# Performance work log

Hardware: AMD Instinct MI355X
Metric: run time of the kernel (lower is better)

Reference implementation:

```python
import jax, jax.numpy as jnp
import numpy as np

B, S, D = 4, 2048, 768
H = 12
DH = D // H
NUM_WAY = 4
DFF = 4 * D  # FFN expansion scale=4
EPS = 1e-6


def setup_inputs() -> dict:
    key = jax.random.key(0)
    ks = jax.random.split(key, 20)
    s = 0.02
    inp = {
        "x": jax.random.normal(ks[0], (B, S, D), jnp.float32),
        "w": jax.random.randint(ks[1], (B, S), 0, NUM_WAY, jnp.int64),
        # LayerNorm 1
        "ln1_g": jnp.ones((D,), jnp.float32),
        "ln1_b": jnp.zeros((D,), jnp.float32),
        # Multi-head attention projections (input_dim=out_dim=D)
        "wq": jax.random.normal(ks[2], (D, D), jnp.float32) * s,
        "bq": jnp.zeros((D,), jnp.float32),
        "wk": jax.random.normal(ks[3], (D, D), jnp.float32) * s,
        "bk": jnp.zeros((D,), jnp.float32),
        "wv": jax.random.normal(ks[4], (D, D), jnp.float32) * s,
        "bv": jnp.zeros((D,), jnp.float32),
        "wo": jax.random.normal(ks[5], (D, D), jnp.float32) * s,
        "bo": jnp.zeros((D,), jnp.float32),
        # Way classifier
        "wcls": jax.random.normal(ks[6], (D, NUM_WAY), jnp.float32) * s,
        "bcls": jnp.zeros((NUM_WAY,), jnp.float32),
        # num_way stacked FFN experts: Linear(D,4D) -> ReLU -> Linear(4D,D)
        "w1": jax.random.normal(ks[7], (NUM_WAY, D, DFF), jnp.float32) * s,
        "b1": jnp.zeros((NUM_WAY, DFF), jnp.float32),
        "w2": jax.random.normal(ks[8], (NUM_WAY, DFF, D), jnp.float32) * s,
        "b2": jnp.zeros((NUM_WAY, D), jnp.float32),
    }
    return inp


def _layernorm(x, g, b):
    mu = jnp.mean(x, axis=-1, keepdims=True)
    var = jnp.mean(jnp.square(x - mu), axis=-1, keepdims=True)
    return (x - mu) * jax.lax.rsqrt(var + EPS) * g + b


def reference(x, w, ln1_g, ln1_b, wq, bq, wk, bk, wv, bv, wo, bo,
              wcls, bcls, w1, b1, w2, b2):
    # pre-LN
    xn = _layernorm(x, ln1_g, ln1_b)
    # multi-head self-attention (q = k = v = xn)
    q = (xn @ wq + bq).reshape(B, S, H, DH)
    k = (xn @ wk + bk).reshape(B, S, H, DH)
    v = (xn @ wv + bv).reshape(B, S, H, DH)
    scores = jnp.einsum('bqhd,bkhd->bhqk', q, k) / jnp.sqrt(jnp.float32(DH))
    attn = jax.nn.softmax(scores, axis=-1)
    ctx = jnp.einsum('bhqk,bkhd->bqhd', attn, v).reshape(B, S, D)
    ctx = ctx @ wo + bo
    # dropout is identity at inference; residual
    out = ctx + x
    # dense compute-all-experts FFN, then per-token select by routing id w
    # (mask-overwrite in original == one-hot select since masks partition)
    ffn_out = jnp.zeros_like(out)
    for ci in range(NUM_WAY):
        h = jax.nn.relu(out @ w1[ci] + b1[ci])        # [B,S,4D]
        fi = h @ w2[ci] + b2[ci]                      # [B,S,D]
        mask = (w == ci).astype(out.dtype)[..., None]  # [B,S,1]
        if ci == 0:
            # original initializes ffn_out with way-0 output everywhere;
            # later ways overwrite where w == ci, net = select expert w
            ffn_out = fi
        else:
            ffn_out = ffn_out * (1.0 - mask) + fi * mask
    way_logits = out @ wcls + bcls  # [B,S,NUM_WAY]
    return ffn_out, way_logits
```

## Files before the change

### kernel.cpp

```cpp
#include <hip/hip_runtime.h>
#include <cstdint>

typedef unsigned short u16;
typedef float f32x4 __attribute__((ext_vector_type(4)));
typedef float f32x16 __attribute__((ext_vector_type(16)));
typedef __bf16 bf16x8 __attribute__((ext_vector_type(8)));

#define LOG2E 1.44269504088896340736f

__device__ __forceinline__ u16 f2bf(float f) {
    union { float f; unsigned u; } v; v.f = f;
    unsigned r = v.u + 0x7fffu + ((v.u >> 16) & 1u);
    return (u16)(r >> 16);
}

__device__ __forceinline__ float bf2f(u16 v) {
    union { unsigned u; float f; } x; x.u = ((unsigned)v) << 16; return x.f;
}

__device__ __forceinline__ unsigned cvt_pk_bf16(float lo, float hi) {
    unsigned r;
    asm("v_cvt_pk_bf16_f32 %0, %1, %2" : "=v"(r) : "v"(lo), "v"(hi));
    return r;
}

__device__ __forceinline__ float exp2_hw(float x) {
    float r;
    asm("v_exp_f32 %0, %1" : "=v"(r) : "v"(x));
    return r;
}

__device__ __forceinline__ f32x4 mfma16(bf16x8 a, bf16x8 b, f32x4 c) {
    return __builtin_amdgcn_mfma_f32_16x16x32_bf16(a, b, c, 0, 0, 0);
}

__device__ __forceinline__ f32x16 mfma32(bf16x8 a, bf16x8 b, f32x16 c) {
    return __builtin_amdgcn_mfma_f32_32x32x16_bf16(a, b, c, 0, 0, 0);
}

__device__ __forceinline__ void gload_lds16(const void* g, void* l) {
    __builtin_amdgcn_global_load_lds(
        (__attribute__((address_space(1))) unsigned int*)(g),
        (__attribute__((address_space(3))) unsigned int*)(l),
        16, 0, 0);
}

#define MB_TOK 8192
#define DM 768
#define HH 12
#define DHD 64
#define NWAY 4
#define DFF 3072
#define SEQ 2048
#define NBATCH 4

#define PREP_LN_END   8192
#define PREP_T7_END   10496
#define PREP_W1_END   19712
#define PREP_W2_END   28928
#define PREP_CB_END   28937
#define PREP_GRID     28938

__global__ __launch_bounds__(256) void prep_kernel(
    const float* __restrict__ x, const float* __restrict__ ln_g,
    const float* __restrict__ ln_b, u16* __restrict__ xn,
    const float* __restrict__ wq, const float* __restrict__ wk,
    const float* __restrict__ wvv, const float* __restrict__ wo,
    u16* __restrict__ wqkvt, u16* __restrict__ wot,
    const float* __restrict__ w1, u16* __restrict__ w1t,
    const float* __restrict__ w2, u16* __restrict__ w2t,
    const float* __restrict__ bq, const float* __restrict__ bk,
    const float* __restrict__ bv, float* __restrict__ bqkv,
    const int* __restrict__ wl, int* __restrict__ perm,
    int* __restrict__ eoff, int4* __restrict__ fmap, int4* __restrict__ fmap64)
{
    __shared__ float tl[32][33];
    __shared__ float red[4];
    __shared__ int cnt[4], cur[4], off[5];
    int bid = blockIdx.x, tid = threadIdx.x;

    if (bid < PREP_LN_END) {
        int row = bid;
        const float* xr = x + (size_t)row * DM;
        float v0 = xr[tid], v1 = xr[tid + 256], v2 = xr[tid + 512];
        float s = v0 + v1 + v2;
        #pragma unroll
        for (int k = 1; k < 64; k <<= 1) s += __shfl_xor(s, k);
        if ((tid & 63) == 0) red[tid >> 6] = s;
        __syncthreads();
        float mu = (red[0] + red[1] + red[2] + red[3]) * (1.f / 768.f);
        float d0 = v0 - mu, d1 = v1 - mu, d2 = v2 - mu;
        float q = d0 * d0 + d1 * d1 + d2 * d2;
        #pragma unroll
        for (int k = 1; k < 64; k <<= 1) q += __shfl_xor(q, k);
        __syncthreads();
        if ((tid & 63) == 0) red[tid >> 6] = q;
        __syncthreads();
        float var = (red[0] + red[1] + red[2] + red[3]) * (1.f / 768.f);
        float rs = rsqrtf(var + 1e-6f);
        u16* xo = xn + (size_t)row * DM;
        xo[tid]       = f2bf(d0 * rs * ln_g[tid]       + ln_b[tid]);
        xo[tid + 256] = f2bf(d1 * rs * ln_g[tid + 256] + ln_b[tid + 256]);
        xo[tid + 512] = f2bf(d2 * rs * ln_g[tid + 512] + ln_b[tid + 512]);
        return;
    }
    if (bid < PREP_W2_END) {
        const float* src; u16* dst; int K, N, n0, k0;
        if (bid < PREP_T7_END) {
            int r = bid - PREP_LN_END;
            int wsel = r / 576, lb = r % 576;
            K = 768; N = 768;
            n0 = (lb % 24) * 32; k0 = (lb / 24) * 32;
            src = wsel == 0 ? wq : (wsel == 1 ? wk : (wsel == 2 ? wvv : wo));
            dst = wsel == 3 ? wot : (wqkvt + (size_t)wsel * 768 * 768);
        } else if (bid < PREP_W1_END) {
            int lb = bid - PREP_T7_END;
            K = 768; N = 3072;
            n0 = (lb % 96) * 32; k0 = ((lb / 96) % 24) * 32;
            int z = lb / 2304;
            src = w1 + (size_t)z * K * N; dst = w1t + (size_t)z * K * N;
        } else {
            int lb = bid - PREP_W1_END;
            K = 3072; N = 768;
            n0 = (lb % 24) * 32; k0 = ((lb / 24) % 96) * 32;
            int z = lb / 2304;
            src = w2 + (size_t)z * K * N; dst = w2t + (size_t)z * K * N;
        }
        int tx = tid & 31, ty = tid >> 5;
        #pragma unroll
        for (int j = 0; j < 4; ++j)
            tl[ty + j * 8][tx] = src[(size_t)(k0 + ty + j * 8) * N + n0 + tx];
        __syncthreads();
        #pragma unroll
        for (int j = 0; j < 4; ++j)
            dst[(size_t)(n0 + ty + j * 8) * K + k0 + tx] = f2bf(tl[tx][ty + j * 8]);
        return;
    }
    if (bid < PREP_CB_END) {
        int i = (bid - PREP_W2_END) * 256 + tid;
        if (i < 2304)
            bqkv[i] = i < 768 ? bq[i] : (i < 1536 ? bk[i - 768] : bv[i - 1536]);
        return;
    }
    if (tid < 4) cnt[tid] = 0;
    __syncthreads();
    for (int t = tid; t < MB_TOK; t += 256) atomicAdd(&cnt[wl[t] & 3], 1);
    __syncthreads();
    if (tid == 0) {
        off[0] = 0;
        for (int e = 0; e < 4; ++e) off[e + 1] = off[e] + cnt[e];
        int idx = 0;
        for (int e = 0; e < 4; ++e)
            for (int s = 0; s < cnt[e]; s += 128)
                fmap[idx++] = make_int4(e, off[e], s, cnt[e] - s);
        for (; idx < 72; ++idx) fmap[idx] = make_int4(-1, 0, 0, 0);
        int idx2 = 0;
        for (int e = 0; e < 4; ++e)
            for (int s = 0; s < cnt[e]; s += 64)
                fmap64[idx2++] = make_int4(e, off[e], s, cnt[e] - s);
        for (; idx2 < 136; ++idx2) fmap64[idx2] = make_int4(-1, 0, 0, 0);
        for (int e = 0; e < 5; ++e) eoff[e] = off[e];
        for (int e = 0; e < 4; ++e) cur[e] = off[e];
    }
    __syncthreads();
    for (int t = tid; t < MB_TOK; t += 256) {
        int e = wl[t] & 3;
        int pos = atomicAdd(&cur[e], 1);
        perm[pos] = t;
    }
}

__global__ __launch_bounds__(256) void vT_kernel(
    const u16* __restrict__ qkv, u16* __restrict__ vT)
{
    __shared__ u16 tl[32][33];
    int bh = blockIdx.z;
    int b = bh / HH, h = bh % HH;
    int key0 = blockIdx.x * 32;
    int d0 = blockIdx.y * 32;
    int tx = threadIdx.x & 31, ty = threadIdx.x >> 5;
    const u16* src = qkv + ((size_t)b * SEQ + key0) * 2304 + 1536 + h * 64 + d0;
    #pragma unroll
    for (int j = 0; j < 4; ++j)
        tl[ty + j * 8][tx] = src[(size_t)(ty + j * 8) * 2304 + tx];
    __syncthreads();
    u16* dst = vT + ((size_t)bh * 64 + d0) * SEQ + key0;
    #pragma unroll
    for (int j = 0; j < 4; ++j)
        dst[(size_t)(ty + j * 8) * SEQ + tx] = tl[tx][ty + j * 8];
}

template<int MODE, int TM, bool RELU, bool RES, bool ST32, bool ST16>
__global__ __launch_bounds__(256, 4) void gemm_bt_kernel(
    const u16* __restrict__ A, const u16* __restrict__ Bt,
    const float* __restrict__ bias, const float* __restrict__ res,
    float* __restrict__ out32, u16* __restrict__ out16,
    int nbt, int N, int K, int ntn,
    const int* __restrict__ perm, const int4* __restrict__ fmap)
{
    constexpr int ALD = TM * 32;
    constexpr int NN  = (TM == 64) ? 2 : 4;
    __shared__ __attribute__((aligned(16))) u16 As[2][ALD];
    __shared__ __attribute__((aligned(16))) u16 Bs[2][4096];
    int tid = threadIdx.x;
    int wv = tid >> 6, ln = tid & 63;
    int bpx = gridDim.x / (ntn << 3);
    int jj = blockIdx.x >> 3;
    int bt = (blockIdx.x & 7) * bpx + jj / ntn;
    int tn = (jj % ntn) * 128;
    if (bt >= nbt) return;

    int seg = 0, ms = 0, mb = TM, tm = 0;
    if (MODE != 0) {
        int4 ent = fmap[bt];
        if (ent.x < 0) return;
        seg = ent.y; ms = ent.z; mb = ent.w; if (mb > TM) mb = TM;
        Bt += (size_t)ent.x * N * K;
        bias += ent.x * N;
    } else {
        tm = bt * TM;
    }

    f32x4 acc[4][NN];
    #pragma unroll
    for (int i = 0; i < 4; ++i)
        #pragma unroll
        for (int j = 0; j < NN; ++j) acc[i][j] = f32x4{0.f, 0.f, 0.f, 0.f};

    int wr = (TM == 128) ? (wv >> 1) : 0;
    int wcol0 = (TM == 128) ? (wv & 1) * 64 : wv * 32;
    int lr = ln & 15, hi = ln >> 4;
    int nk = K / 32;

    const u16* asrc[2];
    const u16* bsrc[2];
    #pragma unroll
    for (int i = 0; i < 2; ++i) {
        int rA = (TM == 128) ? ((wv * 2 + i) * 16 + (ln >> 2))
                             : (wv * 16 + (ln >> 2));
        if (TM == 128 || i == 0) {
            int am = rA < mb ? rA : (mb - 1);
            size_t arow;
            if (MODE == 1)      arow = (size_t)perm[seg + ms + am];
            else if (MODE == 2) arow = (size_t)(seg + ms + am);
            else                arow = (size_t)(tm + rA);
            asrc[i] = A + arow * K + (ln & 3) * 8;
        }
        int rB = (wv * 2 + i) * 16 + (ln >> 2);
        bsrc[i] = Bt + (size_t)(tn + rB) * K + (ln & 3) * 8;
    }
    int aofs0 = (TM == 128) ? (wv * 2) * 512 : wv * 512;

#define GSTAGE(bf_, k0_) do {                                             \
    gload_lds16(asrc[0] + (k0_), &As[bf_][aofs0]);                        \
    if (TM == 128) gload_lds16(asrc[1] + (k0_), &As[bf_][aofs0 + 512]);   \
    gload_lds16(bsrc[0] + (k0_), &Bs[bf_][(wv * 2) * 512]);               \
    gload_lds16(bsrc[1] + (k0_), &Bs[bf_][(wv * 2 + 1) * 512]);           \
} while (0)

    GSTAGE(0, 0);
    for (int kk = 0; kk < nk; ++kk) {
        int bf = kk & 1;
        __syncthreads();
        if (kk + 1 < nk) GSTAGE(bf ^ 1, (kk + 1) * 32);
        bf16x8 a[4], b[NN];
        #pragma unroll
        for (int m = 0; m < 4; ++m)
            a[m] = *(const bf16x8*)&As[bf][(wr * 64 + m * 16 + lr) * 32 + hi * 8];
        #pragma unroll
        for (int n = 0; n < NN; ++n)
            b[n] = *(const bf16x8*)&Bs[bf][(wcol0 + n * 16 + lr) * 32 + hi * 8];
        #pragma unroll
        for (int m = 0; m < 4; ++m)
            #pragma unroll
            for (int n = 0; n < NN; ++n)
                acc[m][n] = mfma16(a[m], b[n], acc[m][n]);
    }
#undef GSTAGE

    #pragma unroll
    for (int m = 0; m < 4; ++m) {
        int rb = wr * 64 + m * 16 + hi * 4;
        #pragma unroll
        for (int n = 0; n < NN; ++n) {
            int gcol = tn + wcol0 + n * 16 + lr;
            float bvv = bias[gcol];
            #pragma unroll
            for (int i = 0; i < 4; ++i) {
                int rml = rb + i;
                float v = acc[m][n][i] + bvv;
                if (RELU) v = v > 0.f ? v : 0.f;
                if (MODE == 0) {
                    size_t grow = (size_t)(tm + rml);
                    if (RES) v += res[grow * N + gcol];
                    if (ST32) out32[grow * N + gcol] = v;
                    if (ST16) out16[grow * N + gcol] = f2bf(v);
                } else {
                    if (rml < mb) {
                        size_t orow = (MODE == 1) ? (size_t)(seg + ms + rml)
                                                  : (size_t)perm[seg + ms + rml];
                        if (ST32) out32[orow * N + gcol] = v;
                        if (ST16) out16[orow * N + gcol] = f2bf(v);
                    }
                }
            }
        }
    }
}

__global__ __launch_bounds__(256, 4) void attn_kernel(
    const u16* __restrict__ qkv, const u16* __restrict__ vT,
    u16* __restrict__ ctx)
{
    __shared__ __attribute__((aligned(16))) u16 Ks[2][4096];
    __shared__ __attribute__((aligned(16))) u16 Vs[2][4096];
    int tid = threadIdx.x;
    int wv = tid >> 6, ln = tid & 63;
    int qv = ln & 31, hi = ln >> 5;
    int bid = blockIdx.x;
    int bh = (bid & 7) * 6 + ((bid >> 3) % 6);
    int qt = (bid >> 3) / 6;
    int b = bh / HH, h = bh % HH;
    int q0 = qt * 128 + wv * 32;
    size_t qrowb = (size_t)(b * SEQ + q0);
    const float C = 0.125f * LOG2E;

    bf16x8 qf[4];
    {
        const u16* qp = qkv + (qrowb + qv) * 2304 + h * 64 + hi * 8;
        #pragma unroll
        for (int ds = 0; ds < 4; ++ds) qf[ds] = *(const bf16x8*)(qp + ds * 16);
    }

    int csrc = 8 * ((ln & 7) ^ (ln >> 3));
    const size_t kbase = (size_t)b * SEQ * 2304 + 768 + h * 64;
    const u16* vtb = vT + (size_t)bh * 64 * SEQ;
    const u16* kp0 = qkv + kbase + (size_t)(wv * 16 + (ln >> 3)) * 2304 + csrc;
    const u16* kp1 = kp0 + (size_t)8 * 2304;
    const u16* vp0 = vtb + (size_t)(wv * 16 + (ln >> 3)) * SEQ + csrc;
    const u16* vp1 = vp0 + (size_t)8 * SEQ;

#define ATTN_STAGE(bf_, t_) do {                                          \
    gload_lds16(kp0 + (size_t)(t_) * 64 * 2304, &Ks[bf_][(wv * 2) * 512]);\
    gload_lds16(kp1 + (size_t)(t_) * 64 * 2304, &Ks[bf_][(wv * 2 + 1) * 512]);\
    gload_lds16(vp0 + (size_t)(t_) * 64, &Vs[bf_][(wv * 2) * 512]);       \
    gload_lds16(vp1 + (size_t)(t_) * 64, &Vs[bf_][(wv * 2 + 1) * 512]);   \
} while (0)

    f32x16 oacc[2];
    #pragma unroll
    for (int i = 0; i < 2; ++i)
        #pragma unroll
        for (int r = 0; r < 16; ++r) oacc[i][r] = 0.f;
    float m_run = -INFINITY, l_run = 0.f;
    int ksw = (qv & 7) * 8;

    ATTN_STAGE(0, 0);

    for (int kt = 0; kt < SEQ / 64; ++kt) {
        int bf = kt & 1;
        __syncthreads();
        if (kt + 1 < SEQ / 64) ATTN_STAGE(bf ^ 1, kt + 1);

        f32x16 s0, s1;
        #pragma unroll
        for (int r = 0; r < 16; ++r) { s0[r] = 0.f; s1[r] = 0.f; }
        #pragma unroll
        for (int ds = 0; ds < 4; ++ds) {
            bf16x8 ka0 = *(const bf16x8*)&Ks[bf][qv * 64 + ((ds * 16 + hi * 8) ^ ksw)];
            bf16x8 ka1 = *(const bf16x8*)&Ks[bf][(32 + qv) * 64 + ((ds * 16 + hi * 8) ^ ksw)];
            s0 = mfma32(ka0, qf[ds], s0);
            s1 = mfma32(ka1, qf[ds], s1);
        }

        float tmax = s0[0];
        #pragma unroll
        for (int r = 1; r < 16; ++r) tmax = fmaxf(tmax, s0[r]);
        #pragma unroll
        for (int r = 0; r < 16; ++r) tmax = fmaxf(tmax, s1[r]);
        tmax = fmaxf(tmax, __shfl_xor(tmax, 32));

        if (!__all(tmax - m_run <= 64.f)) {
            float m_new = fmaxf(m_run, tmax);
            float corr = exp2_hw((m_run - m_new) * C);
            l_run *= corr;
            #pragma unroll
            for (int i = 0; i < 2; ++i)
                #pragma unroll
                for (int r = 0; r < 16; ++r) oacc[i][r] *= corr;
            m_run = m_new;
        }
        float c2 = -m_run * C;
        float psum = 0.f;
        #pragma unroll
        for (int r = 0; r < 16; ++r) {
            s0[r] = exp2_hw(fmaf(s0[r], C, c2)); psum += s0[r];
            s1[r] = exp2_hw(fmaf(s1[r], C, c2)); psum += s1[r];
        }
        l_run += psum;

        #pragma unroll
        for (int kb = 0; kb < 2; ++kb) {
            #pragma unroll
            for (int hc = 0; hc < 2; ++hc) {
                const f32x16& sv = kb ? s1 : s0;
                unsigned x0 = cvt_pk_bf16(sv[8 * hc + 0], sv[8 * hc + 1]);
                unsigned x1 = cvt_pk_bf16(sv[8 * hc + 2], sv[8 * hc + 3]);
                unsigned x2 = cvt_pk_bf16(sv[8 * hc + 4], sv[8 * hc + 5]);
                unsigned x3 = cvt_pk_bf16(sv[8 * hc + 6], sv[8 * hc + 7]);
                unsigned t0 = hi ? x0 : x2, t1 = hi ? x1 : x3;
                unsigned r0 = (unsigned)__shfl_xor((int)t0, 32);
                unsigned r1 = (unsigned)__shfl_xor((int)t1, 32);
                union { bf16x8 v; unsigned u[4]; } pf;
                pf.u[0] = hi ? r0 : x0; pf.u[1] = hi ? r1 : x1;
                pf.u[2] = hi ? x2 : r0; pf.u[3] = hi ? x3 : r1;
                int kc = (kb * 32 + hc * 16 + hi * 8) ^ ksw;
                #pragma unroll
                for (int dblk = 0; dblk < 2; ++dblk) {
                    bf16x8 va = *(const bf16x8*)&Vs[bf][(dblk * 32 + qv) * 64 + kc];
                    oacc[dblk] = mfma32(va, pf.v, oacc[dblk]);
                }
            }
        }
    }
#undef ATTN_STAGE

    float l_tot = l_run + __shfl_xor(l_run, 32);
    float inv = 1.f / l_tot;

    __syncthreads();
    u16* eb = &Ks[0][0] + wv * 2048;
    #pragma unroll
    for (int dblk = 0; dblk < 2; ++dblk)
        #pragma unroll
        for (int r = 0; r < 16; r += 2) {
            int d = dblk * 32 + (r & 3) + 8 * (r >> 2) + 4 * hi;
            unsigned pk = cvt_pk_bf16(oacc[dblk][r] * inv, oacc[dblk][r + 1] * inv);
            *(unsigned*)&eb[qv * 64 + (d ^ ((qv & 7) * 8))] = pk;
        }
    __syncthreads();
    {
        u16* ctr = ctx + (qrowb + qv) * DM + h * 64 + hi * 32;
        #pragma unroll
        for (int g = 0; g < 4; ++g) {
            bf16x8 vv = *(const bf16x8*)&eb[qv * 64 + ((hi * 32 + g * 8) ^ ((qv & 7) * 8))];
            *(bf16x8*)(ctr + g * 8) = vv;
        }
    }
}

__global__ __launch_bounds__(256) void cls_kernel(
    const u16* __restrict__ outm, const float* __restrict__ wcls,
    const float* __restrict__ bcls, float* __restrict__ dst)
{
    int row = blockIdx.x, t = threadIdx.x;
    const u16* xr = outm + (size_t)row * DM;
    float a0 = 0, a1 = 0, a2 = 0, a3 = 0;
    for (int j = t; j < DM; j += 256) {
        float xv = bf2f(xr[j]);
        float4 wv4 = *(const float4*)(const void*)(wcls + (size_t)j * 4);
        a0 += xv * wv4.x; a1 += xv * wv4.y; a2 += xv * wv4.z; a3 += xv * wv4.w;
    }
    #pragma unroll
    for (int k = 1; k < 64; k <<= 1) {
        a0 += __shfl_xor(a0, k); a1 += __shfl_xor(a1, k);
        a2 += __shfl_xor(a2, k); a3 += __shfl_xor(a3, k);
    }
    __shared__ float red[4][4];
    if ((t & 63) == 0) {
        int wid = t >> 6;
        red[wid][0] = a0; red[wid][1] = a1; red[wid][2] = a2; red[wid][3] = a3;
    }
    __syncthreads();
    if (t < 4)
        dst[(size_t)row * 4 + t] =
            red[0][t] + red[1][t] + red[2][t] + red[3][t] + bcls[t];
}

extern "C" void kernel_launch(void* const* d_in, const int* in_sizes, int n_in,
                              void* d_out, int out_size, void* d_ws, size_t ws_size,
                              hipStream_t stream) {
    const float* x      = (const float*)d_in[0];
    const int*   wl     = (const int*)d_in[1];
    const float* ln_g   = (const float*)d_in[2];
    const float* ln_b   = (const float*)d_in[3];
    const float* wq     = (const float*)d_in[4];
    const float* bq     = (const float*)d_in[5];
    const float* wk     = (const float*)d_in[6];
    const float* bk     = (const float*)d_in[7];
    const float* wvv    = (const float*)d_in[8];
    const float* bv     = (const float*)d_in[9];
    const float* wo     = (const float*)d_in[10];
    const float* bo     = (const float*)d_in[11];
    const float* wcls   = (const float*)d_in[12];
    const float* bcls   = (const float*)d_in[13];
    const float* w1     = (const float*)d_in[14];
    const float* b1     = (const float*)d_in[15];
    const float* w2     = (const float*)d_in[16];
    const float* b2     = (const float*)d_in[17];
    float* out = (float*)d_out;

    char* ws = (char*)d_ws;
    u16*   xn    = (u16*)  (ws + 0);
    u16*   qkv   = (u16*)  (ws + 12582912);
    u16*   hbuf  = (u16*)  (ws + 0);
    u16*   ctx   = (u16*)  (ws + 50331648);
    u16*   outb  = (u16*)  (ws + 62914560);
    u16*   wqkvt = (u16*)  (ws + 75497472);
    u16*   wot   = (u16*)  (ws + 79036416);
    u16*   w1t   = (u16*)  (ws + 80216064);
    u16*   w2t   = (u16*)  (ws + 99090432);
    float* bqkv  = (float*)(ws + 117964800);
    int*   perm  = (int*)  (ws + 117974016);
    int*   eoff  = (int*)  (ws + 118006784);
    int4*  fmap  = (int4*) (ws + 118006816);
    int4*  fmap64= (int4*) (ws + 118007968);
    u16*   vT    = (u16*)  (ws + 118010144);

    prep_kernel<<<PREP_GRID, 256, 0, stream>>>(
        x, ln_g, ln_b, xn, wq, wk, wvv, wo, wqkvt, wot,
        w1, w1t, w2, w2t, bq, bk, bv, bqkv, wl, perm, eoff, fmap, fmap64);

    gemm_bt_kernel<0, 128, false, false, false, true><<<1152, 256, 0, stream>>>(
        xn, wqkvt, bqkv, nullptr, nullptr, qkv, 64, 2304, 768, 18, nullptr, nullptr);

    vT_kernel<<<dim3(64, 2, 48), 256, 0, stream>>>(qkv, vT);

    attn_kernel<<<768, 256, 0, stream>>>(qkv, vT, ctx);

    gemm_bt_kernel<0, 64, false, true, false, true><<<768, 256, 0, stream>>>(
        ctx, wot, bo, x, nullptr, outb, 128, 768, 768, 6, nullptr, nullptr);

    cls_kernel<<<MB_TOK, 256, 0, stream>>>(outb, wcls, bcls, out + (size_t)MB_TOK * DM);

    gemm_bt_kernel<1, 128, true, false, false, true><<<1728, 256, 0, stream>>>(
        outb, w1t, b1, nullptr, nullptr, hbuf, 72, DFF, 768, 24, perm, fmap);

    gemm_bt_kernel<2, 64, false, false, true, false><<<816, 256, 0, stream>>>(
        hbuf, w2t, b2, nullptr, out, nullptr, 136, 768, DFF, 6, perm, fmap64);
}
```

Baseline: 357.7 us.

## Split-K the second expert FFN GEMM with atomic accumulation

Adds a split-K template parameter to the GEMM and uses two K slices for the down-projection GEMM (K=3072), doubling its grid and merging partial sums into the fp32 output with unsafe atomic adds. The output is zeroed with a memset first, and only the first slice adds the bias. Launch-bounds occupancy hints are also raised. The aim is better CU occupancy on a grid of only 816 blocks, at the cost of atomic traffic, an extra memset and a nondeterministic summation order.

```diff
diff --git a/kernel.cpp b/kernel.cpp
--- a/kernel.cpp
+++ b/kernel.cpp
@@ -190,8 +190,8 @@
         dst[(size_t)(ty + j * 8) * SEQ + tx] = tl[tx][ty + j * 8];
 }
 
-template<int MODE, int TM, bool RELU, bool RES, bool ST32, bool ST16>
-__global__ __launch_bounds__(256, 4) void gemm_bt_kernel(
+template<int MODE, int TM, int KS, bool RELU, bool RES, bool ST32, bool ST16>
+__global__ __launch_bounds__(256, (TM == 64) ? 6 : 5) void gemm_bt_kernel(
     const u16* __restrict__ A, const u16* __restrict__ Bt,
     const float* __restrict__ bias, const float* __restrict__ res,
     float* __restrict__ out32, u16* __restrict__ out16,
@@ -204,10 +204,13 @@
     __shared__ __attribute__((aligned(16))) u16 Bs[2][4096];
     int tid = threadIdx.x;
     int wv = tid >> 6, ln = tid & 63;
-    int bpx = gridDim.x / (ntn << 3);
+    int per = ntn * KS;
+    int bpx = gridDim.x / (per << 3);
     int jj = blockIdx.x >> 3;
-    int bt = (blockIdx.x & 7) * bpx + jj / ntn;
-    int tn = (jj % ntn) * 128;
+    int bt = (blockIdx.x & 7) * bpx + jj / per;
+    int rem = jj % per;
+    int tn = (rem % ntn) * 128;
+    int ks = rem / ntn;
     if (bt >= nbt) return;
 
     int seg = 0, ms = 0, mb = TM, tm = 0;
@@ -230,7 +233,8 @@
     int wr = (TM == 128) ? (wv >> 1) : 0;
     int wcol0 = (TM == 128) ? (wv & 1) * 64 : wv * 32;
     int lr = ln & 15, hi = ln >> 4;
-    int nk = K / 32;
+    int nk = K / KS / 32;
+    int kbase = ks * (K / KS);
 
     const u16* asrc[2];
     const u16* bsrc[2];
@@ -244,10 +248,10 @@
             if (MODE == 1)      arow = (size_t)perm[seg + ms + am];
             else if (MODE == 2) arow = (size_t)(seg + ms + am);
             else                arow = (size_t)(tm + rA);
-            asrc[i] = A + arow * K + (ln & 3) * 8;
+            asrc[i] = A + arow * K + kbase + (ln & 3) * 8;
         }
         int rB = (wv * 2 + i) * 16 + (ln >> 2);
-        bsrc[i] = Bt + (size_t)(tn + rB) * K + (ln & 3) * 8;
+        bsrc[i] = Bt + (size_t)(tn + rB) * K + kbase + (ln & 3) * 8;
     }
     int aofs0 = (TM == 128) ? (wv * 2) * 512 : wv * 512;
 
@@ -284,7 +288,7 @@
         #pragma unroll
         for (int n = 0; n < NN; ++n) {
             int gcol = tn + wcol0 + n * 16 + lr;
-            float bvv = bias[gcol];
+            float bvv = (KS > 1 && ks != 0) ? 0.f : bias[gcol];
             #pragma unroll
             for (int i = 0; i < 4; ++i) {
                 int rml = rb + i;
@@ -299,7 +303,10 @@
                     if (rml < mb) {
                         size_t orow = (MODE == 1) ? (size_t)(seg + ms + rml)
                                                   : (size_t)perm[seg + ms + rml];
-                        if (ST32) out32[orow * N + gcol] = v;
+                        if (ST32) {
+                            if (KS > 1) unsafeAtomicAdd(&out32[orow * N + gcol], v);
+                            else        out32[orow * N + gcol] = v;
+                        }
                         if (ST16) out16[orow * N + gcol] = f2bf(v);
                     }
                 }
@@ -517,25 +524,27 @@
     int4*  fmap64= (int4*) (ws + 118007968);
     u16*   vT    = (u16*)  (ws + 118010144);
 
+    hipMemsetAsync(out, 0, (size_t)MB_TOK * DM * sizeof(float), stream);
+
     prep_kernel<<<PREP_GRID, 256, 0, stream>>>(
         x, ln_g, ln_b, xn, wq, wk, wvv, wo, wqkvt, wot,
         w1, w1t, w2, w2t, bq, bk, bv, bqkv, wl, perm, eoff, fmap, fmap64);
 
-    gemm_bt_kernel<0, 128, false, false, false, true><<<1152, 256, 0, stream>>>(
+    gemm_bt_kernel<0, 128, 1, false, false, false, true><<<1152, 256, 0, stream>>>(
         xn, wqkvt, bqkv, nullptr, nullptr, qkv, 64, 2304, 768, 18, nullptr, nullptr);
 
     vT_kernel<<<dim3(64, 2, 48), 256, 0, stream>>>(qkv, vT);
 
     attn_kernel<<<768, 256, 0, stream>>>(qkv, vT, ctx);
 
-    gemm_bt_kernel<0, 64, false, true, false, true><<<768, 256, 0, stream>>>(
+    gemm_bt_kernel<0, 64, 1, false, true, false, true><<<768, 256, 0, stream>>>(
         ctx, wot, bo, x, nullptr, outb, 128, 768, 768, 6, nullptr, nullptr);
 
     cls_kernel<<<MB_TOK, 256, 0, stream>>>(outb, wcls, bcls, out + (size_t)MB_TOK * DM);
 
-    gemm_bt_kernel<1, 128, true, false, false, true><<<1728, 256, 0, stream>>>(
+    gemm_bt_kernel<1, 128, 1, true, false, false, true><<<1728, 256, 0, stream>>>(
         outb, w1t, b1, nullptr, nullptr, hbuf, 72, DFF, 768, 24, perm, fmap);
 
-    gemm_bt_kernel<2, 64, false, false, true, false><<<816, 256, 0, stream>>>(
+    gemm_bt_kernel<2, 64, 2, false, false, true, false><<<1632, 256, 0, stream>>>(
         hbuf, w2t, b2, nullptr, out, nullptr, 136, 768, DFF, 6, perm, fmap64);
 }
```

Result: slower. 416.8 us (+16.5%).

## Triple-buffer GEMM LDS stages with explicit vmcnt waits and inline ds_read

Applied to the files above, without the earlier changes.

Moves the bt GEMM K-loop from double to triple buffering in LDS. Global-to-LDS loads are issued two stages ahead, and the full __syncthreads is replaced by a partial s_waitcnt vmcnt plus a raw s_barrier. LDS fragment reads switch to inline-asm ds_read_b128 with precomputed byte offsets, and sched_barriers separate the reads from the MFMA block. The extra buffer raises LDS usage, so the TM=128 launch bound drops to 3 blocks per CU. Correctness now depends on the hand-counted vmcnt values.

```diff
diff --git a/kernel.cpp b/kernel.cpp
--- a/kernel.cpp
+++ b/kernel.cpp
@@ -5,6 +5,7 @@
 typedef float f32x4 __attribute__((ext_vector_type(4)));
 typedef float f32x16 __attribute__((ext_vector_type(16)));
 typedef __bf16 bf16x8 __attribute__((ext_vector_type(8)));
+typedef unsigned u32x4v __attribute__((ext_vector_type(4)));
 
 #define LOG2E 1.44269504088896340736f
 
@@ -43,6 +44,16 @@
         (__attribute__((address_space(1))) unsigned int*)(g),
         (__attribute__((address_space(3))) unsigned int*)(l),
         16, 0, 0);
+}
+
+__device__ __forceinline__ unsigned lds_off(const void* p) {
+    return (unsigned)(size_t)(__attribute__((address_space(3))) const void*)p;
+}
+
+__device__ __forceinline__ bf16x8 lds_read16(unsigned byte_off) {
+    u32x4v r;
+    asm volatile("ds_read_b128 %0, %1" : "=v"(r) : "v"(byte_off));
+    union { u32x4v u; bf16x8 b; } c; c.u = r; return c.b;
 }
 
 #define MB_TOK 8192
@@ -191,7 +202,7 @@
 }
 
 template<int MODE, int TM, bool RELU, bool RES, bool ST32, bool ST16>
-__global__ __launch_bounds__(256, 4) void gemm_bt_kernel(
+__global__ __launch_bounds__(256, (TM == 64) ? 4 : 3) void gemm_bt_kernel(
     const u16* __restrict__ A, const u16* __restrict__ Bt,
     const float* __restrict__ bias, const float* __restrict__ res,
     float* __restrict__ out32, u16* __restrict__ out16,
@@ -200,8 +211,9 @@
 {
     constexpr int ALD = TM * 32;
     constexpr int NN  = (TM == 64) ? 2 : 4;
-    __shared__ __attribute__((aligned(16))) u16 As[2][ALD];
-    __shared__ __attribute__((aligned(16))) u16 Bs[2][4096];
+    constexpr int NLD = (TM == 128) ? 4 : 3;
+    __shared__ __attribute__((aligned(16))) u16 As[3][ALD];
+    __shared__ __attribute__((aligned(16))) u16 Bs[3][4096];
     int tid = threadIdx.x;
     int wv = tid >> 6, ln = tid & 63;
     int bpx = gridDim.x / (ntn << 3);
@@ -251,30 +263,47 @@
     }
     int aofs0 = (TM == 128) ? (wv * 2) * 512 : wv * 512;
 
-#define GSTAGE(bf_, k0_) do {                                             \
-    gload_lds16(asrc[0] + (k0_), &As[bf_][aofs0]);                        \
-    if (TM == 128) gload_lds16(asrc[1] + (k0_), &As[bf_][aofs0 + 512]);   \
-    gload_lds16(bsrc[0] + (k0_), &Bs[bf_][(wv * 2) * 512]);               \
-    gload_lds16(bsrc[1] + (k0_), &Bs[bf_][(wv * 2 + 1) * 512]);           \
+    unsigned abase = lds_off(&As[0][0]);
+    unsigned bbase = lds_off(&Bs[0][0]);
+    unsigned aro = (unsigned)(((wr * 64 + lr) * 32 + hi * 8) * 2);
+    unsigned bro = (unsigned)(((wcol0 + lr) * 32 + hi * 8) * 2);
+
+#define GSTAGE(b_, k0_) do {                                              \
+    gload_lds16(asrc[0] + (k0_), &As[b_][aofs0]);                         \
+    if (TM == 128) gload_lds16(asrc[1] + (k0_), &As[b_][aofs0 + 512]);    \
+    gload_lds16(bsrc[0] + (k0_), &Bs[b_][(wv * 2) * 512]);                \
+    gload_lds16(bsrc[1] + (k0_), &Bs[b_][(wv * 2 + 1) * 512]);            \
 } while (0)
 
     GSTAGE(0, 0);
+    GSTAGE(1, 32);
+    int bf3 = 0;
     for (int kk = 0; kk < nk; ++kk) {
-        int bf = kk & 1;
-        __syncthreads();
-        if (kk + 1 < nk) GSTAGE(bf ^ 1, (kk + 1) * 32);
+        if (kk + 1 < nk)
+            asm volatile("s_waitcnt vmcnt(%0)" :: "i"(NLD) : "memory");
+        else
+            asm volatile("s_waitcnt vmcnt(0)" ::: "memory");
+        __builtin_amdgcn_s_barrier();
+        __builtin_amdgcn_sched_barrier(0);
+        if (kk + 2 < nk) {
+            int nb = bf3 + 2; if (nb >= 3) nb -= 3;
+            GSTAGE(nb, (kk + 2) * 32);
+        }
+        unsigned ab = abase + (unsigned)(bf3 * (ALD * 2)) + aro;
+        unsigned bb = bbase + (unsigned)(bf3 * 8192) + bro;
         bf16x8 a[4], b[NN];
         #pragma unroll
-        for (int m = 0; m < 4; ++m)
-            a[m] = *(const bf16x8*)&As[bf][(wr * 64 + m * 16 + lr) * 32 + hi * 8];
-        #pragma unroll
-        for (int n = 0; n < NN; ++n)
-            b[n] = *(const bf16x8*)&Bs[bf][(wcol0 + n * 16 + lr) * 32 + hi * 8];
+        for (int m = 0; m < 4; ++m) a[m] = lds_read16(ab + m * 1024);
+        #pragma unroll
+        for (int n = 0; n < NN; ++n) b[n] = lds_read16(bb + n * 1024);
+        asm volatile("s_waitcnt lgkmcnt(0)" ::: "memory");
+        __builtin_amdgcn_sched_barrier(0);
         #pragma unroll
         for (int m = 0; m < 4; ++m)
             #pragma unroll
             for (int n = 0; n < NN; ++n)
                 acc[m][n] = mfma16(a[m], b[n], acc[m][n]);
+        bf3 = (bf3 == 2) ? 0 : bf3 + 1;
     }
 #undef GSTAGE
 
```

Result: no change. 361.1 us (+0.9%).
